# Performance work log

Hardware: AMD Instinct MI355X
Metric: run time of the kernel (lower is better)

## Reference

```python
import jax, jax.numpy as jnp
import numpy as np

N = 50000      # nodes
E = 800000     # edges (avg degree 16)
IN = 256       # in_feats
H = 256        # hidden_size
HEADS = 4
DH = H // HEADS  # 64
SCALE = np.sqrt(DH).astype(np.float32)


def _lin_init(k, fan_in, fan_out):
    s = 1.0 / np.sqrt(fan_in)
    k1, k2 = jax.random.split(k)
    W = jax.random.uniform(k1, (fan_in, fan_out), jnp.float32, -s, s)
    b = jax.random.uniform(k2, (fan_out,), jnp.float32, -s, s)
    return W, b


def setup_inputs() -> dict:
    key = jax.random.key(0)
    ks = jax.random.split(key, 20)
    d = {}
    d["features"] = jax.random.normal(ks[0], (N, IN), jnp.float32)
    d["src"] = jax.random.randint(ks[1], (E,), 0, N)
    d["dst"] = jax.random.randint(ks[2], (E,), 0, N)
    d["edge_types"] = jax.random.randint(ks[3], (E,), 0, 4)
    d["Wm"], d["bm"] = _lin_init(ks[4], IN, H)
    i = 5
    for l in (1, 2, 3):
        for nm in ("Q", "K", "V"):
            d[f"W{nm}{l}"], d[f"b{nm}{l}"] = _lin_init(ks[i], H, H)
            i += 1
    d["W1"], d["b1"] = _lin_init(ks[i], 3 * H, 2 * H); i += 1
    d["W2"], d["b2"] = _lin_init(ks[i], 2 * H, H); i += 1
    d["W3"], d["b3"] = _lin_init(ks[i], H, 1)
    return d


def _norms(src, dst):
    # DGL GraphConv norm='both': src normalized by out-degree, dst by in-degree
    ones = jnp.ones((E,), jnp.float32)
    deg_out = jax.ops.segment_sum(ones, src, num_segments=N)
    deg_in = jax.ops.segment_sum(ones, dst, num_segments=N)
    ns = jnp.where(deg_out > 0, deg_out ** -0.5, 0.0)[:, None]  # [N,1]
    nd = jnp.where(deg_in > 0, deg_in ** -0.5, 0.0)[:, None]
    return ns, nd


def _gcn(x, W, b, src, dst, ns, nd):
    # h = D_in^{-1/2} A D_out^{-1/2} x W + b
    m = (x * ns)[src]                                   # [E,H] gather
    agg = jax.ops.segment_sum(m, dst, num_segments=N)   # [N,H] scatter-sum
    return (agg * nd) @ W + b


def _attn(x, WQ, bQ, WK, bK, WV, bV, src, dst, ns, nd):
    Q = jax.nn.relu(_gcn(x, WQ, bQ, src, dst, ns, nd)).reshape(N, HEADS, DH)
    K = jax.nn.relu(_gcn(x, WK, bK, src, dst, ns, nd)).reshape(N, HEADS, DH)
    V = jax.nn.relu(_gcn(x, WV, bV, src, dst, ns, nd)).reshape(N, HEADS, DH)
    # edge scores: src K dot dst Q, scaled exp with clamp
    score = jnp.exp(jnp.clip((K[src] * Q[dst]).sum(-1) / SCALE, -10.0, 10.0))  # [E,HEADS]
    wV = jax.ops.segment_sum(V[src] * score[:, :, None], dst, num_segments=N)  # [N,HEADS,DH]
    z = jax.ops.segment_sum(score, dst, num_segments=N)                        # [N,HEADS]
    return (wV / (z[:, :, None] + 1e-6)).reshape(N, H)


def reference(features, src, dst, edge_types, Wm, bm,
              WQ1, bQ1, WK1, bK1, WV1, bV1,
              WQ2, bQ2, WK2, bK2, WV2, bV2,
              WQ3, bQ3, WK3, bK3, WV3, bV3,
              W1, b1, W2, b2, W3, b3):
    ns, nd = _norms(src, dst)
    x = jax.nn.relu(features @ Wm + bm)
    x1 = _attn(x, WQ1, bQ1, WK1, bK1, WV1, bV1, src, dst, ns, nd)
    x2 = _attn(x1, WQ2, bQ2, WK2, bK2, WV2, bV2, src, dst, ns, nd)
    x3 = _attn(x2, WQ3, bQ3, WK3, bK3, WV3, bV3, src, dst, ns, nd)
    x = jnp.concatenate((x1, x2, x3), axis=1)          # [N, 3H]
    x = jax.nn.relu(x @ W1 + b1)
    x = jax.nn.relu(x @ W2 + b2)
    x = (x @ W3 + b3)[:, 0]
    return jax.nn.sigmoid(x)
```

## Files before the change

### kernel.cpp

```cpp
#include <hip/hip_runtime.h>
#include <stdint.h>

#define NN 50000
#define NE 800000

typedef float f32x4 __attribute__((ext_vector_type(4)));
typedef short s16x8 __attribute__((ext_vector_type(8)));

__device__ __forceinline__ float bf2f(unsigned short u) {
    union { unsigned int i; float f; } v; v.i = ((unsigned int)u) << 16; return v.f;
}
__device__ __forceinline__ unsigned short f2bf(float x) {
    union { float f; unsigned int i; } v; v.f = x;
    unsigned int r = v.i + 0x7FFFu + ((v.i >> 16) & 1u);
    return (unsigned short)(r >> 16);
}


__global__ void k_deg(const int* __restrict__ src, const int* __restrict__ dst,
                      int* __restrict__ dego, int* __restrict__ degi) {
    int e = blockIdx.x * 256 + threadIdx.x;
    if (e < NE) {
        atomicAdd(&dego[src[e]], 1);
        atomicAdd(&degi[dst[e]], 1);
    }
}

__global__ void k_norm(const int* __restrict__ dego, const int* __restrict__ degi,
                       float* __restrict__ ns, float* __restrict__ nd) {
    int i = blockIdx.x * 256 + threadIdx.x;
    if (i < NN) {
        ns[i] = dego[i] > 0 ? rsqrtf((float)dego[i]) : 0.f;
        nd[i] = degi[i] > 0 ? rsqrtf((float)degi[i]) : 0.f;
    }
}

__global__ void k_scan(const int* __restrict__ deg, int* __restrict__ row_ptr,
                       int* __restrict__ cursor) {
    __shared__ int tmp[1024];
    __shared__ int carry_s;
    if (threadIdx.x == 0) carry_s = 0;
    __syncthreads();
    for (int base = 0; base < NN; base += 1024) {
        int i = base + (int)threadIdx.x;
        int v = (i < NN) ? deg[i] : 0;
        int c = carry_s;
        tmp[threadIdx.x] = v;
        __syncthreads();
        int sum = v;
        for (int off = 1; off < 1024; off <<= 1) {
            int t = (threadIdx.x >= (unsigned)off) ? tmp[threadIdx.x - off] : 0;
            __syncthreads();
            sum += t;
            tmp[threadIdx.x] = sum;
            __syncthreads();
        }
        if (i < NN) { int ex = c + sum - v; row_ptr[i] = ex; cursor[i] = ex; }
        __syncthreads();
        if (threadIdx.x == 0) carry_s = c + tmp[1023];
        __syncthreads();
    }
    if (threadIdx.x == 0) row_ptr[NN] = carry_s;
}

__global__ void k_fill(const int* __restrict__ src, const int* __restrict__ dst,
                       int* __restrict__ cursor, int* __restrict__ col_src) {
    int e = blockIdx.x * 256 + threadIdx.x;
    if (e < NE) {
        int slot = atomicAdd(&cursor[dst[e]], 1);
        col_src[slot] = src[e];
    }
}

__global__ void k_wsplit(const float* __restrict__ W, unsigned short* __restrict__ hi,
                         unsigned short* __restrict__ lo, int K, int Ncols) {
    int idx = blockIdx.x * 256 + threadIdx.x;
    if (idx < K * Ncols) {
        int n = idx / K, k = idx - n * K;
        float w = W[(size_t)k * Ncols + n];
        unsigned short h = f2bf(w);
        hi[idx] = h;
        lo[idx] = f2bf(w - bf2f(h));
    }
}


__global__ void k_prop(const float* __restrict__ x, int ldx,
                       const int* __restrict__ row_ptr, const int* __restrict__ col_src,
                       const float* __restrict__ ns, const float* __restrict__ ndv,
                       float* __restrict__ y) {
    int w = (int)((blockIdx.x * 256 + threadIdx.x) >> 6);
    if (w >= NN) return;
    int lane = threadIdx.x & 63;
    int c = lane * 4;
    float a0 = 0, a1 = 0, a2 = 0, a3 = 0;
    int e0 = row_ptr[w], e1 = row_ptr[w + 1];
    for (int p = e0; p < e1; ++p) {
        int s = col_src[p];
        float wgt = ns[s];
        const float4 xv = *(const float4*)(x + (size_t)s * ldx + c);
        a0 += wgt * xv.x; a1 += wgt * xv.y; a2 += wgt * xv.z; a3 += wgt * xv.w;
    }
    float sc = ndv[w];
    float4 o; o.x = a0 * sc; o.y = a1 * sc; o.z = a2 * sc; o.w = a3 * sc;
    *(float4*)(y + (size_t)w * 256 + c) = o;
}


__global__ void k_attn(const float* __restrict__ QKV,
                       const int* __restrict__ row_ptr, const int* __restrict__ col_src,
                       float* __restrict__ xo) {
    int w = (int)((blockIdx.x * 256 + threadIdx.x) >> 6);
    if (w >= NN) return;
    int lane = threadIdx.x & 63;
    int c = lane * 4;
    const float4 q = *(const float4*)(QKV + (size_t)w * 768 + c);
    float v0 = 0, v1 = 0, v2 = 0, v3 = 0, z = 0;
    int e0 = row_ptr[w], e1 = row_ptr[w + 1];
    for (int p = e0; p < e1; ++p) {
        int s = col_src[p];
        const float4 kk = *(const float4*)(QKV + (size_t)s * 768 + 256 + c);
        float t = q.x * kk.x + q.y * kk.y + q.z * kk.z + q.w * kk.w;
        t += __shfl_xor(t, 1);
        t += __shfl_xor(t, 2);
        t += __shfl_xor(t, 4);
        t += __shfl_xor(t, 8);
        float scv = __expf(fminf(fmaxf(t * 0.125f, -10.f), 10.f));
        const float4 vv = *(const float4*)(QKV + (size_t)s * 768 + 512 + c);
        v0 += scv * vv.x; v1 += scv * vv.y; v2 += scv * vv.z; v3 += scv * vv.w;
        z += scv;
    }
    float inv = 1.f / (z + 1e-6f);
    float4 o; o.x = v0 * inv; o.y = v1 * inv; o.z = v2 * inv; o.w = v3 * inv;
    *(float4*)(xo + (size_t)w * 768 + c) = o;
}


__global__ __launch_bounds__(256) void k_gemm(
    const float* __restrict__ A, int lda,
    const unsigned short* __restrict__ Bhi, const unsigned short* __restrict__ Blo,
    const float* __restrict__ bias,
    float* __restrict__ C, int ldc, int coff, int M, int K) {
    __shared__ unsigned short sA[2][128][40];
    __shared__ unsigned short sB[2][128][40];
    const int tid = threadIdx.x;
    const int lane = tid & 63;
    const int wid = tid >> 6;
    const int wm = wid & 1, wn = wid >> 1;
    const int fr = lane & 15, kg = lane >> 4;
    const int brow = blockIdx.x * 128;
    const int bcol = blockIdx.y * 128;
    f32x4 acc[4][4] = {};

    for (int k0 = 0; k0 < K; k0 += 32) {
#pragma unroll
        for (int rep = 0; rep < 2; ++rep) {
            int s = tid + rep * 256;
            int row = s >> 2, ks = (s & 3) * 8;
            int gr = brow + row;
            float4 f0 = make_float4(0, 0, 0, 0), f1 = make_float4(0, 0, 0, 0);
            if (gr < M) {
                const float4* ap = (const float4*)(A + (size_t)gr * lda + k0 + ks);
                f0 = ap[0];
                f1 = ap[1];
            }
            ushort4 h0, h1v, l0, l1v;
            h0.x = f2bf(f0.x); l0.x = f2bf(f0.x - bf2f(h0.x));
            h0.y = f2bf(f0.y); l0.y = f2bf(f0.y - bf2f(h0.y));
            h0.z = f2bf(f0.z); l0.z = f2bf(f0.z - bf2f(h0.z));
            h0.w = f2bf(f0.w); l0.w = f2bf(f0.w - bf2f(h0.w));
            h1v.x = f2bf(f1.x); l1v.x = f2bf(f1.x - bf2f(h1v.x));
            h1v.y = f2bf(f1.y); l1v.y = f2bf(f1.y - bf2f(h1v.y));
            h1v.z = f2bf(f1.z); l1v.z = f2bf(f1.z - bf2f(h1v.z));
            h1v.w = f2bf(f1.w); l1v.w = f2bf(f1.w - bf2f(h1v.w));
            *(ushort4*)&sA[0][row][ks] = h0;
            *(ushort4*)&sA[0][row][ks + 4] = h1v;
            *(ushort4*)&sA[1][row][ks] = l0;
            *(ushort4*)&sA[1][row][ks + 4] = l1v;
            size_t bbase = (size_t)(bcol + row) * K + k0 + ks;
            *(uint4*)&sB[0][row][ks] = *(const uint4*)(Bhi + bbase);
            *(uint4*)&sB[1][row][ks] = *(const uint4*)(Blo + bbase);
        }
        __syncthreads();
        s16x8 ah[4], al[4], bh[4], bl[4];
#pragma unroll
        for (int f = 0; f < 4; ++f) {
            ah[f] = *(const s16x8*)&sA[0][wm * 64 + f * 16 + fr][kg * 8];
            al[f] = *(const s16x8*)&sA[1][wm * 64 + f * 16 + fr][kg * 8];
            bh[f] = *(const s16x8*)&sB[0][wn * 64 + f * 16 + fr][kg * 8];
            bl[f] = *(const s16x8*)&sB[1][wn * 64 + f * 16 + fr][kg * 8];
        }
#pragma unroll
        for (int i = 0; i < 4; ++i)
#pragma unroll
            for (int j = 0; j < 4; ++j) {
                acc[i][j] = __builtin_amdgcn_mfma_f32_16x16x32_bf16(ah[i], bh[j], acc[i][j], 0, 0, 0);
                acc[i][j] = __builtin_amdgcn_mfma_f32_16x16x32_bf16(ah[i], bl[j], acc[i][j], 0, 0, 0);
                acc[i][j] = __builtin_amdgcn_mfma_f32_16x16x32_bf16(al[i], bh[j], acc[i][j], 0, 0, 0);
            }
        __syncthreads();
    }

#pragma unroll
    for (int i = 0; i < 4; ++i) {
#pragma unroll
        for (int j = 0; j < 4; ++j) {
            int colL = bcol + wn * 64 + j * 16 + fr;
            float bb = bias[colL];
#pragma unroll
            for (int r = 0; r < 4; ++r) {
                int row = brow + wm * 64 + i * 16 + kg * 4 + r;
                if (row < M) {
                    C[(size_t)row * ldc + coff + colL] = fmaxf(acc[i][j][r] + bb, 0.f);
                }
            }
        }
    }
}


__global__ void k_final(const float* __restrict__ h2, const float* __restrict__ W3,
                        const float* __restrict__ b3, float* __restrict__ out) {
    int w = (int)((blockIdx.x * 256 + threadIdx.x) >> 6);
    if (w >= NN) return;
    int lane = threadIdx.x & 63;
    float4 h = *(const float4*)(h2 + (size_t)w * 256 + lane * 4);
    float4 ww = *(const float4*)(W3 + lane * 4);
    float p = h.x * ww.x + h.y * ww.y + h.z * ww.z + h.w * ww.w;
    p += __shfl_xor(p, 1);
    p += __shfl_xor(p, 2);
    p += __shfl_xor(p, 4);
    p += __shfl_xor(p, 8);
    p += __shfl_xor(p, 16);
    p += __shfl_xor(p, 32);
    if (lane == 0) out[w] = 1.f / (1.f + __expf(-(p + b3[0])));
}

__global__ void k_sent(float* __restrict__ out) {
    int i = blockIdx.x * 256 + threadIdx.x;
    if (i < NN) out[i] = 0.5f;
}


extern "C" void kernel_launch(void* const* d_in, const int* in_sizes, int n_in,
                              void* d_out, int out_size, void* d_ws, size_t ws_size,
                              hipStream_t stream) {
    const float* features = (const float*)d_in[0];
    const int* src = (const int*)d_in[1];
    const int* dst = (const int*)d_in[2];
    const float* Wm = (const float*)d_in[4];
    const float* bm = (const float*)d_in[5];
    const float* Wq[3] = {(const float*)d_in[6], (const float*)d_in[12], (const float*)d_in[18]};
    const float* bq[3] = {(const float*)d_in[7], (const float*)d_in[13], (const float*)d_in[19]};
    const float* Wk[3] = {(const float*)d_in[8], (const float*)d_in[14], (const float*)d_in[20]};
    const float* bk[3] = {(const float*)d_in[9], (const float*)d_in[15], (const float*)d_in[21]};
    const float* Wv[3] = {(const float*)d_in[10], (const float*)d_in[16], (const float*)d_in[22]};
    const float* bv[3] = {(const float*)d_in[11], (const float*)d_in[17], (const float*)d_in[23]};
    const float* W1 = (const float*)d_in[24];
    const float* b1 = (const float*)d_in[25];
    const float* W2 = (const float*)d_in[26];
    const float* b2 = (const float*)d_in[27];
    const float* W3 = (const float*)d_in[28];
    const float* b3 = (const float*)d_in[29];
    float* out = (float*)d_out;

    char* ws = (char*)d_ws;
    size_t off = 0;
    auto alloc = [&](size_t b) -> void* {
        void* p = ws + off;
        off = (off + b + 255) & ~(size_t)255;
        return p;
    };

    int* deg_o = (int*)alloc(NN * 4);
    int* deg_i = (int*)alloc(NN * 4);
    int* row_ptr = (int*)alloc((NN + 1) * 4);
    int* cursor = (int*)alloc(NN * 4);
    int* col_src = (int*)alloc((size_t)NE * 4);
    float* ns = (float*)alloc(NN * 4);
    float* nd = (float*)alloc(NN * 4);

    unsigned short* Wmt_h = (unsigned short*)alloc(256 * 256 * 2);
    unsigned short* Wmt_l = (unsigned short*)alloc(256 * 256 * 2);
    unsigned short *Wqkvt_h[3][3], *Wqkvt_l[3][3];
    for (int l = 0; l < 3; ++l)
        for (int m = 0; m < 3; ++m) {
            Wqkvt_h[l][m] = (unsigned short*)alloc(256 * 256 * 2);
            Wqkvt_l[l][m] = (unsigned short*)alloc(256 * 256 * 2);
        }
    unsigned short* W1t_h = (unsigned short*)alloc(512 * 768 * 2);
    unsigned short* W1t_l = (unsigned short*)alloc(512 * 768 * 2);
    unsigned short* W2t_h = (unsigned short*)alloc(256 * 512 * 2);
    unsigned short* W2t_l = (unsigned short*)alloc(256 * 512 * 2);

    float* QKV = (float*)alloc((size_t)NN * 768 * 4);
    float* y = (float*)alloc((size_t)NN * 256 * 4);
    float* xcat = (float*)alloc((size_t)NN * 768 * 4);

    float* x0 = QKV;
    float* h1 = QKV;
    float* h2 = y;

    (void)in_sizes; (void)n_in; (void)out_size;

    if (off > ws_size) {
        k_sent<<<(NN + 255) / 256, 256, 0, stream>>>(out);
        return;
    }

    hipMemsetAsync(deg_o, 0, NN * 4, stream);
    hipMemsetAsync(deg_i, 0, NN * 4, stream);
    k_deg<<<(NE + 255) / 256, 256, 0, stream>>>(src, dst, deg_o, deg_i);
    k_norm<<<(NN + 255) / 256, 256, 0, stream>>>(deg_o, deg_i, ns, nd);
    k_scan<<<1, 1024, 0, stream>>>(deg_i, row_ptr, cursor);
    k_fill<<<(NE + 255) / 256, 256, 0, stream>>>(src, dst, cursor, col_src);

    k_wsplit<<<(256 * 256 + 255) / 256, 256, 0, stream>>>(Wm, Wmt_h, Wmt_l, 256, 256);
    for (int l = 0; l < 3; ++l) {
        k_wsplit<<<(256 * 256 + 255) / 256, 256, 0, stream>>>(Wq[l], Wqkvt_h[l][0], Wqkvt_l[l][0], 256, 256);
        k_wsplit<<<(256 * 256 + 255) / 256, 256, 0, stream>>>(Wk[l], Wqkvt_h[l][1], Wqkvt_l[l][1], 256, 256);
        k_wsplit<<<(256 * 256 + 255) / 256, 256, 0, stream>>>(Wv[l], Wqkvt_h[l][2], Wqkvt_l[l][2], 256, 256);
    }
    k_wsplit<<<(768 * 512 + 255) / 256, 256, 0, stream>>>(W1, W1t_h, W1t_l, 768, 512);
    k_wsplit<<<(512 * 256 + 255) / 256, 256, 0, stream>>>(W2, W2t_h, W2t_l, 512, 256);

    const int MB = (NN + 127) / 128;
    dim3 gN256(MB, 2), gN512(MB, 4);

    k_gemm<<<gN256, 256, 0, stream>>>(features, 256, Wmt_h, Wmt_l, bm,
                                      x0, 256, 0, NN, 256);

    const float* xin = x0;
    int ldx = 256;
    for (int l = 0; l < 3; ++l) {
        k_prop<<<12500, 256, 0, stream>>>(xin, ldx, row_ptr, col_src, ns, nd, y);
        k_gemm<<<gN256, 256, 0, stream>>>(y, 256, Wqkvt_h[l][0], Wqkvt_l[l][0], bq[l],
                                          QKV, 768, 0, NN, 256);
        k_gemm<<<gN256, 256, 0, stream>>>(y, 256, Wqkvt_h[l][1], Wqkvt_l[l][1], bk[l],
                                          QKV, 768, 256, NN, 256);
        k_gemm<<<gN256, 256, 0, stream>>>(y, 256, Wqkvt_h[l][2], Wqkvt_l[l][2], bv[l],
                                          QKV, 768, 512, NN, 256);
        k_attn<<<12500, 256, 0, stream>>>(QKV, row_ptr, col_src, xcat + 256 * l);
        xin = xcat + 256 * l;
        ldx = 768;
    }

    k_gemm<<<gN512, 256, 0, stream>>>(xcat, 768, W1t_h, W1t_l, b1, h1, 512, 0, NN, 768);
    k_gemm<<<gN256, 256, 0, stream>>>(h1, 512, W2t_h, W2t_l, b2, h2, 256, 0, NN, 512);
    k_final<<<12500, 256, 0, stream>>>(h2, W3, b3, out);
}
```

Before: 9.918 us.

## Fuse QKV GEMMs, parallelize degree scan, batch weight splits, prefetch gather indices

Replaces the single-block serial prefix scan with a three-kernel multi-block scan. Concatenates the Q/K/V weights per layer into one transposed bf16 hi/lo buffer, produced by one batched split kernel, and concatenates the biases. This lets each layer run one wide GEMM instead of three. The prop and attention gather loops now prefetch the next neighbor index and issue the K and V loads together to hide latency. Together these cut launch count and serial work, at the cost of extra scan kernels and more live registers.

```diff
diff --git a/kernel.cpp b/kernel.cpp
--- a/kernel.cpp
+++ b/kernel.cpp
@@ -3,6 +3,7 @@
 
 #define NN 50000
 #define NE 800000
+#define NBLK 196
 
 typedef float f32x4 __attribute__((ext_vector_type(4)));
 typedef short s16x8 __attribute__((ext_vector_type(8)));
@@ -35,32 +36,51 @@
     }
 }
 
-__global__ void k_scan(const int* __restrict__ deg, int* __restrict__ row_ptr,
-                       int* __restrict__ cursor) {
-    __shared__ int tmp[1024];
-    __shared__ int carry_s;
-    if (threadIdx.x == 0) carry_s = 0;
+__global__ void k_scanA(const int* __restrict__ deg, int* __restrict__ incl,
+                        int* __restrict__ bsum) {
+    __shared__ int sm[256];
+    int t = threadIdx.x, i = blockIdx.x * 256 + t;
+    int v = (i < NN) ? deg[i] : 0;
+    sm[t] = v;
     __syncthreads();
-    for (int base = 0; base < NN; base += 1024) {
-        int i = base + (int)threadIdx.x;
-        int v = (i < NN) ? deg[i] : 0;
-        int c = carry_s;
-        tmp[threadIdx.x] = v;
-        __syncthreads();
-        int sum = v;
-        for (int off = 1; off < 1024; off <<= 1) {
-            int t = (threadIdx.x >= (unsigned)off) ? tmp[threadIdx.x - off] : 0;
-            __syncthreads();
-            sum += t;
-            tmp[threadIdx.x] = sum;
-            __syncthreads();
-        }
-        if (i < NN) { int ex = c + sum - v; row_ptr[i] = ex; cursor[i] = ex; }
-        __syncthreads();
-        if (threadIdx.x == 0) carry_s = c + tmp[1023];
-        __syncthreads();
-    }
-    if (threadIdx.x == 0) row_ptr[NN] = carry_s;
+#pragma unroll
+    for (int off = 1; off < 256; off <<= 1) {
+        int tv = (t >= off) ? sm[t - off] : 0;
+        __syncthreads();
+        sm[t] += tv;
+        __syncthreads();
+    }
+    if (i < NN) incl[i] = sm[t];
+    if (t == 255) bsum[blockIdx.x] = sm[255];
+}
+
+__global__ void k_scanB(const int* __restrict__ bsum, int* __restrict__ boff,
+                        int* __restrict__ row_ptr) {
+    __shared__ int sm[256];
+    int t = threadIdx.x;
+    int v = (t < NBLK) ? bsum[t] : 0;
+    sm[t] = v;
+    __syncthreads();
+#pragma unroll
+    for (int off = 1; off < 256; off <<= 1) {
+        int tv = (t >= off) ? sm[t - off] : 0;
+        __syncthreads();
+        sm[t] += tv;
+        __syncthreads();
+    }
+    if (t < NBLK) boff[t] = sm[t] - v;
+    if (t == 255) row_ptr[NN] = sm[255];
+}
+
+__global__ void k_scanC(const int* __restrict__ deg, const int* __restrict__ incl,
+                        const int* __restrict__ boff, int* __restrict__ row_ptr,
+                        int* __restrict__ cursor) {
+    int i = blockIdx.x * 256 + threadIdx.x;
+    if (i < NN) {
+        int ex = boff[blockIdx.x] + incl[i] - deg[i];
+        row_ptr[i] = ex;
+        cursor[i] = ex;
+    }
 }
 
 __global__ void k_fill(const int* __restrict__ src, const int* __restrict__ dst,
@@ -82,6 +102,33 @@
         hi[idx] = h;
         lo[idx] = f2bf(w - bf2f(h));
     }
+}
+
+struct QkvPtrs {
+    const float* w[9];
+    unsigned short* h[3];
+    unsigned short* l[3];
+};
+
+__global__ void k_wsplit9(QkvPtrs P) {
+    int m = blockIdx.y;
+    int layer = m / 3, which = m - layer * 3;
+    int idx = blockIdx.x * 256 + threadIdx.x;
+    int n = idx >> 8, k = idx & 255;
+    float w = P.w[m][(size_t)k * 256 + n];
+    unsigned short h = f2bf(w);
+    size_t o = (size_t)(which * 256 + n) * 256 + k;
+    P.h[layer][o] = h;
+    P.l[layer][o] = f2bf(w - bf2f(h));
+}
+
+struct BiasPtrs { const float* b[9]; float* dst; };
+
+__global__ void k_bcat(BiasPtrs P) {
+    int m = blockIdx.x;
+    int layer = m / 3, which = m - layer * 3;
+    int t = threadIdx.x;
+    P.dst[layer * 768 + which * 256 + t] = P.b[m][t];
 }
 
 
@@ -95,11 +142,14 @@
     int c = lane * 4;
     float a0 = 0, a1 = 0, a2 = 0, a3 = 0;
     int e0 = row_ptr[w], e1 = row_ptr[w + 1];
+    int sv = (e0 < e1) ? col_src[e0] : 0;
+    float wv = (e0 < e1) ? ns[sv] : 0.f;
     for (int p = e0; p < e1; ++p) {
-        int s = col_src[p];
-        float wgt = ns[s];
-        const float4 xv = *(const float4*)(x + (size_t)s * ldx + c);
-        a0 += wgt * xv.x; a1 += wgt * xv.y; a2 += wgt * xv.z; a3 += wgt * xv.w;
+        int sn = 0; float wn = 0.f;
+        if (p + 1 < e1) { sn = col_src[p + 1]; wn = ns[sn]; }
+        const float4 xv = *(const float4*)(x + (size_t)sv * ldx + c);
+        a0 += wv * xv.x; a1 += wv * xv.y; a2 += wv * xv.z; a3 += wv * xv.w;
+        sv = sn; wv = wn;
     }
     float sc = ndv[w];
     float4 o; o.x = a0 * sc; o.y = a1 * sc; o.z = a2 * sc; o.w = a3 * sc;
@@ -117,18 +167,20 @@
     const float4 q = *(const float4*)(QKV + (size_t)w * 768 + c);
     float v0 = 0, v1 = 0, v2 = 0, v3 = 0, z = 0;
     int e0 = row_ptr[w], e1 = row_ptr[w + 1];
+    int sv = (e0 < e1) ? col_src[e0] : 0;
     for (int p = e0; p < e1; ++p) {
-        int s = col_src[p];
-        const float4 kk = *(const float4*)(QKV + (size_t)s * 768 + 256 + c);
+        int sn = (p + 1 < e1) ? col_src[p + 1] : 0;
+        const float4 kk = *(const float4*)(QKV + (size_t)sv * 768 + 256 + c);
+        const float4 vv = *(const float4*)(QKV + (size_t)sv * 768 + 512 + c);
         float t = q.x * kk.x + q.y * kk.y + q.z * kk.z + q.w * kk.w;
         t += __shfl_xor(t, 1);
         t += __shfl_xor(t, 2);
         t += __shfl_xor(t, 4);
         t += __shfl_xor(t, 8);
         float scv = __expf(fminf(fmaxf(t * 0.125f, -10.f), 10.f));
-        const float4 vv = *(const float4*)(QKV + (size_t)s * 768 + 512 + c);
         v0 += scv * vv.x; v1 += scv * vv.y; v2 += scv * vv.z; v3 += scv * vv.w;
         z += scv;
+        sv = sn;
     }
     float inv = 1.f / (z + 1e-6f);
     float4 o; o.x = v0 * inv; o.y = v1 * inv; o.z = v2 * inv; o.w = v3 * inv;
@@ -250,12 +302,6 @@
     const int* dst = (const int*)d_in[2];
     const float* Wm = (const float*)d_in[4];
     const float* bm = (const float*)d_in[5];
-    const float* Wq[3] = {(const float*)d_in[6], (const float*)d_in[12], (const float*)d_in[18]};
-    const float* bq[3] = {(const float*)d_in[7], (const float*)d_in[13], (const float*)d_in[19]};
-    const float* Wk[3] = {(const float*)d_in[8], (const float*)d_in[14], (const float*)d_in[20]};
-    const float* bk[3] = {(const float*)d_in[9], (const float*)d_in[15], (const float*)d_in[21]};
-    const float* Wv[3] = {(const float*)d_in[10], (const float*)d_in[16], (const float*)d_in[22]};
-    const float* bv[3] = {(const float*)d_in[11], (const float*)d_in[17], (const float*)d_in[23]};
     const float* W1 = (const float*)d_in[24];
     const float* b1 = (const float*)d_in[25];
     const float* W2 = (const float*)d_in[26];
@@ -279,15 +325,18 @@
     int* col_src = (int*)alloc((size_t)NE * 4);
     float* ns = (float*)alloc(NN * 4);
     float* nd = (float*)alloc(NN * 4);
+    int* incl = (int*)alloc(NN * 4);
+    int* bsum = (int*)alloc(NBLK * 4);
+    int* boff = (int*)alloc(NBLK * 4);
 
     unsigned short* Wmt_h = (unsigned short*)alloc(256 * 256 * 2);
     unsigned short* Wmt_l = (unsigned short*)alloc(256 * 256 * 2);
-    unsigned short *Wqkvt_h[3][3], *Wqkvt_l[3][3];
-    for (int l = 0; l < 3; ++l)
-        for (int m = 0; m < 3; ++m) {
-            Wqkvt_h[l][m] = (unsigned short*)alloc(256 * 256 * 2);
-            Wqkvt_l[l][m] = (unsigned short*)alloc(256 * 256 * 2);
-        }
+    unsigned short *Wqkvt_h[3], *Wqkvt_l[3];
+    for (int l = 0; l < 3; ++l) {
+        Wqkvt_h[l] = (unsigned short*)alloc(768 * 256 * 2);
+        Wqkvt_l[l] = (unsigned short*)alloc(768 * 256 * 2);
+    }
+    float* bqkv = (float*)alloc(3 * 768 * 4);
     unsigned short* W1t_h = (unsigned short*)alloc(512 * 768 * 2);
     unsigned short* W1t_l = (unsigned short*)alloc(512 * 768 * 2);
     unsigned short* W2t_h = (unsigned short*)alloc(256 * 512 * 2);
@@ -311,21 +360,31 @@
     hipMemsetAsync(deg_o, 0, NN * 4, stream);
     hipMemsetAsync(deg_i, 0, NN * 4, stream);
     k_deg<<<(NE + 255) / 256, 256, 0, stream>>>(src, dst, deg_o, deg_i);
-    k_norm<<<(NN + 255) / 256, 256, 0, stream>>>(deg_o, deg_i, ns, nd);
-    k_scan<<<1, 1024, 0, stream>>>(deg_i, row_ptr, cursor);
+    k_norm<<<NBLK, 256, 0, stream>>>(deg_o, deg_i, ns, nd);
+    k_scanA<<<NBLK, 256, 0, stream>>>(deg_i, incl, bsum);
+    k_scanB<<<1, 256, 0, stream>>>(bsum, boff, row_ptr);
+    k_scanC<<<NBLK, 256, 0, stream>>>(deg_i, incl, boff, row_ptr, cursor);
     k_fill<<<(NE + 255) / 256, 256, 0, stream>>>(src, dst, cursor, col_src);
 
     k_wsplit<<<(256 * 256 + 255) / 256, 256, 0, stream>>>(Wm, Wmt_h, Wmt_l, 256, 256);
+    QkvPtrs qp;
+    BiasPtrs bp;
     for (int l = 0; l < 3; ++l) {
-        k_wsplit<<<(256 * 256 + 255) / 256, 256, 0, stream>>>(Wq[l], Wqkvt_h[l][0], Wqkvt_l[l][0], 256, 256);
-        k_wsplit<<<(256 * 256 + 255) / 256, 256, 0, stream>>>(Wk[l], Wqkvt_h[l][1], Wqkvt_l[l][1], 256, 256);
-        k_wsplit<<<(256 * 256 + 255) / 256, 256, 0, stream>>>(Wv[l], Wqkvt_h[l][2], Wqkvt_l[l][2], 256, 256);
-    }
+        for (int m = 0; m < 3; ++m) {
+            qp.w[l * 3 + m] = (const float*)d_in[6 + l * 6 + m * 2];
+            bp.b[l * 3 + m] = (const float*)d_in[7 + l * 6 + m * 2];
+        }
+        qp.h[l] = Wqkvt_h[l];
+        qp.l[l] = Wqkvt_l[l];
+    }
+    bp.dst = bqkv;
+    k_wsplit9<<<dim3(256, 9), 256, 0, stream>>>(qp);
+    k_bcat<<<9, 256, 0, stream>>>(bp);
     k_wsplit<<<(768 * 512 + 255) / 256, 256, 0, stream>>>(W1, W1t_h, W1t_l, 768, 512);
     k_wsplit<<<(512 * 256 + 255) / 256, 256, 0, stream>>>(W2, W2t_h, W2t_l, 512, 256);
 
     const int MB = (NN + 127) / 128;
-    dim3 gN256(MB, 2), gN512(MB, 4);
+    dim3 gN256(MB, 2), gN512(MB, 4), gN768(MB, 6);
 
     k_gemm<<<gN256, 256, 0, stream>>>(features, 256, Wmt_h, Wmt_l, bm,
                                       x0, 256, 0, NN, 256);
@@ -334,12 +393,8 @@
     int ldx = 256;
     for (int l = 0; l < 3; ++l) {
         k_prop<<<12500, 256, 0, stream>>>(xin, ldx, row_ptr, col_src, ns, nd, y);
-        k_gemm<<<gN256, 256, 0, stream>>>(y, 256, Wqkvt_h[l][0], Wqkvt_l[l][0], bq[l],
+        k_gemm<<<gN768, 256, 0, stream>>>(y, 256, Wqkvt_h[l], Wqkvt_l[l], bqkv + l * 768,
                                           QKV, 768, 0, NN, 256);
-        k_gemm<<<gN256, 256, 0, stream>>>(y, 256, Wqkvt_h[l][1], Wqkvt_l[l][1], bk[l],
-                                          QKV, 768, 256, NN, 256);
-        k_gemm<<<gN256, 256, 0, stream>>>(y, 256, Wqkvt_h[l][2], Wqkvt_l[l][2], bv[l],
-                                          QKV, 768, 512, NN, 256);
         k_attn<<<12500, 256, 0, stream>>>(QKV, row_ptr, col_src, xcat + 256 * l);
         xin = xcat + 256 * l;
         ldx = 768;
```

New measurement: 9.672 us. 2.5% less time.
